# Optimization experiments

Hardware: AMD Instinct MI355X
Metric: run time of the kernel (lower is better)

Reference implementation:

```python
import jax, jax.numpy as jnp
import numpy as np

B, T, D, DFF = 8, 2048, 1024, 4096
EPS = 1e-6
PLIF_ALPHA = 2.0


@jax.custom_vjp
def spike_fn(m):
    # hard threshold forward, atan surrogate backward (PLIF neuron)
    return (m > 0.0).astype(m.dtype)

def _spk_fwd(m):
    return (m > 0.0).astype(m.dtype), m

def _spk_bwd(m, g):
    ds = PLIF_ALPHA / (2.0 * (1.0 + (jnp.pi * 0.5 * PLIF_ALPHA * m) ** 2))
    return (g * ds,)

spike_fn.defvjp(_spk_fwd, _spk_bwd)


def _rmsnorm(x, w):
    rstd = jax.lax.rsqrt(jnp.mean(x * x, axis=-1, keepdims=True) + EPS)
    return x * rstd * w


def setup_inputs() -> dict:
    key = jax.random.key(0)
    ks = jax.random.split(key, 9)
    sc = 0.02
    return {
        'x': jax.random.normal(ks[0], (B, T, D), jnp.float32),
        'rms_w1': jnp.ones((D,), jnp.float32),
        'rms_w2': jnp.ones((D,), jnp.float32),
        'delta_w': sc * jax.random.normal(ks[1], (D, D), jnp.float32),
        'delta_b': jnp.zeros((D,), jnp.float32),
        'b_w': sc * jax.random.normal(ks[2], (D, D), jnp.float32),
        'b_b': jnp.zeros((D,), jnp.float32),
        'A_log': jnp.log(jnp.linspace(0.5, 2.0, D).astype(jnp.float32)),
        'log_tau': jnp.full((D,), jnp.log(2.0), jnp.float32),
        'plif_thr': jnp.ones((D,), jnp.float32),
        'syn_w': sc * jax.random.normal(ks[3], (D, D), jnp.float32),
        'syn_b': jnp.zeros((D,), jnp.float32),
        'gate_w': sc * jax.random.normal(ks[4], (D, D), jnp.float32),
        'gate_b': jnp.zeros((D,), jnp.float32),
        'ffn_g_w': sc * jax.random.normal(ks[5], (DFF, D), jnp.float32),
        'ffn_u_w': sc * jax.random.normal(ks[6], (DFF, D), jnp.float32),
        'ffn_d_w': sc * jax.random.normal(ks[7], (D, DFF), jnp.float32),
    }


def _forward(x, rms_w1, rms_w2, delta_w, delta_b, b_w, b_b, A_log, log_tau,
             plif_thr, syn_w, syn_b, gate_w, gate_b, ffn_g_w, ffn_u_w, ffn_d_w):
    Bx, Tx, Dx = x.shape
    # --- RMSNorm 1 ---
    y1 = _rmsnorm(x, rms_w1)
    # --- selective-scan style liquid inputs ---
    delta = jax.nn.softplus(jnp.einsum('btd,ed->bte', y1, delta_w) + delta_b)  # [B,T,D]
    bvec = delta * (jnp.einsum('btd,ed->bte', y1, b_w) + b_b)                  # [B,T,D]
    A = jnp.exp(-delta * jnp.exp(A_log))                                        # [B,T,D]

    # --- liquid recurrent scan: h_t = tanh(A_t * h_{t-1} + b_t) ---
    def liquid_step(h, ab):
        a_t, b_t = ab
        h = jnp.tanh(a_t * h + b_t)
        return h, h

    h0 = jnp.zeros((Bx, Dx), x.dtype)
    _, h_post = jax.lax.scan(liquid_step, h0,
                             (jnp.swapaxes(A, 0, 1), jnp.swapaxes(bvec, 0, 1)))
    h_post = jnp.swapaxes(h_post, 0, 1)  # [B,T,D]

    # --- PLIF spiking scan with soft reset ---
    pdec = jnp.exp(-1.0 / jnp.exp(log_tau))  # [D]

    def plif_step(v, h_t):
        v_pre = pdec * v + (1.0 - pdec) * h_t
        s = spike_fn(v_pre - plif_thr)
        return v_pre - s * plif_thr, s

    v0 = jnp.zeros((Bx, Dx), x.dtype)
    _, spike = jax.lax.scan(plif_step, v0, jnp.swapaxes(h_post, 0, 1))
    spike = jnp.swapaxes(spike, 0, 1)

    # --- SEW shortcut + synaptic gate ---
    spike_in = spike + h_post
    syn = jnp.einsum('btd,ed->bte', spike_in, syn_w) + syn_b
    gate = jax.nn.sigmoid(jnp.einsum('btd,ed->bte', spike_in, gate_w) + gate_b)
    x1 = x + syn * gate

    # --- RMSNorm 2 + SwiGLU FFN + residual ---
    y2 = _rmsnorm(x1, rms_w2)
    ffn_act = jax.nn.silu(y2 @ ffn_g_w.T) * (y2 @ ffn_u_w.T)
    return x1 + ffn_act @ ffn_d_w.T


def reference(x, rms_w1, rms_w2, delta_w, delta_b, b_w, b_b, A_log, log_tau,
              plif_thr, syn_w, syn_b, gate_w, gate_b, ffn_g_w, ffn_u_w, ffn_d_w):
    return _forward(x, rms_w1, rms_w2, delta_w, delta_b, b_w, b_b, A_log,
                    log_tau, plif_thr, syn_w, syn_b, gate_w, gate_b,
                    ffn_g_w, ffn_u_w, ffn_d_w)
```

## Files before the change

kernel.cpp:

```cpp
#include <hip/hip_runtime.h>
#include <stdint.h>

#define B_   8
#define T_   2048
#define D_   1024
#define DFF_ 4096
#define M_   (B_ * T_)

typedef __bf16 bf16;
typedef bf16  bf16x8 __attribute__((ext_vector_type(8)));
typedef bf16  bf16x4 __attribute__((ext_vector_type(4)));
typedef float f32x4  __attribute__((ext_vector_type(4)));

#define CAST_LDS(p) ((__attribute__((address_space(3))) void*)(p))
#define CAST_GLB(p) ((const __attribute__((address_space(1))) void*)(p))

__global__ void f2bf_kernel(const float* __restrict__ s, bf16* __restrict__ d, int n) {
    int i = (blockIdx.x * 256 + threadIdx.x) * 4;
    if (i >= n) return;
    float4 v = *(const float4*)(s + i);
    bf16x4 o;
    o[0] = (bf16)v.x; o[1] = (bf16)v.y; o[2] = (bf16)v.z; o[3] = (bf16)v.w;
    *(bf16x4*)(d + i) = o;
}

__global__ __launch_bounds__(256) void rmsnorm_kernel(const float* __restrict__ x,
                                                      const float* __restrict__ w,
                                                      bf16* __restrict__ y) {
    const size_t row = blockIdx.x;
    const int t = threadIdx.x;
    const float4 v = ((const float4*)(x + row * D_))[t];
    float ss = v.x * v.x + v.y * v.y + v.z * v.z + v.w * v.w;
#pragma unroll
    for (int off = 32; off; off >>= 1) ss += __shfl_down(ss, off);
    __shared__ float red[4];
    if ((t & 63) == 0) red[t >> 6] = ss;
    __syncthreads();
    const float total = red[0] + red[1] + red[2] + red[3];
    const float rstd = rsqrtf(total * (1.0f / (float)D_) + 1e-6f);
    const float4 wv = ((const float4*)w)[t];
    bf16x4 o;
    o[0] = (bf16)(v.x * rstd * wv.x);
    o[1] = (bf16)(v.y * rstd * wv.y);
    o[2] = (bf16)(v.z * rstd * wv.z);
    o[3] = (bf16)(v.w * rstd * wv.w);
    ((bf16x4*)(y + row * D_))[t] = o;
}

#define SCAN_C  16
#define SCAN_L  (T_ / SCAN_C)
#define SCAN_W  64
#define SCAN_PF 8

template <int N, int W0>
__device__ __forceinline__ void scan_body(const uint32_t* __restrict__ p,
                                          bf16* __restrict__ o, const int ts,
                                          const float pdec, const float om,
                                          const float th) {
    uint32_t buf[SCAN_PF];
#pragma unroll
    for (int i = 0; i < SCAN_PF; ++i) buf[i] = p[(size_t)i * D_];
    float h = 0.0f, v = 0.0f;
#pragma unroll 8
    for (int k = 0; k < N; ++k) {
        const uint32_t w = buf[k & (SCAN_PF - 1)];
        if (k + SCAN_PF < N) buf[k & (SCAN_PF - 1)] = p[(size_t)(k + SCAN_PF) * D_];
        const float a  = __builtin_bit_cast(float, w << 16);
        const float bb = __builtin_bit_cast(float, w & 0xffff0000u);
        const float xv = fmaf(a, h, bb);
        const float e2 = __expf(2.0f * xv);
        h = 1.0f - __fdividef(2.0f, 1.0f + e2);
        const float vpre = fmaf(pdec, v, om * h);
        const float s = (vpre > th) ? 1.0f : 0.0f;
        v = vpre - s * th;
        if (k >= W0) o[(size_t)(ts + k) * D_] = (bf16)(s + h);
    }
}

__global__ __launch_bounds__(256) void scan_kernel(const uint32_t* __restrict__ ABp,
                                                   const float* __restrict__ log_tau,
                                                   const float* __restrict__ thr,
                                                   bf16* __restrict__ sp) {
    const int g = blockIdx.x * 256 + threadIdx.x;
    const int d = g & (D_ - 1);
    const int bc = g >> 10;
    const int b = bc >> 4;
    const int c = bc & (SCAN_C - 1);
    const float pdec = __expf(-__expf(-log_tau[d]));
    const float om = 1.0f - pdec;
    const float th = thr[d];
    const int t0 = c * SCAN_L;
    const uint32_t* base = ABp + (size_t)b * (T_ * D_) + d;
    bf16* o = sp + (size_t)b * (T_ * D_) + d;
    if (c == 0) {
        scan_body<SCAN_L, 0>(base, o, 0, pdec, om, th);
    } else {
        const int ts = t0 - SCAN_W;
        scan_body<SCAN_L + SCAN_W, SCAN_W>(base + (size_t)ts * D_, o, ts, pdec, om, th);
    }
}

template <int NB, int MODE>
__global__ __launch_bounds__(256, 2) void gemm_kernel(
    const bf16* __restrict__ A, const bf16* __restrict__ W1, const bf16* __restrict__ W2,
    const int M, const int N, const int K,
    const float* __restrict__ b1, const float* __restrict__ b2,
    const float* __restrict__ extra, void* __restrict__ outp) {
    __shared__ bf16 As[128 * 32];
    __shared__ bf16 Bs[NB][128 * 32];

    const int tid = threadIdx.x;
    const int wave = tid >> 6;
    const int lane = tid & 63;
    const int lane15 = lane & 15;
    const int quad = lane >> 4;
    const int m0 = blockIdx.y * 128;
    const int n0 = blockIdx.x * 128;
    const int wm = (wave >> 1) * 64;
    const int wn = (wave & 1) * 64;

    f32x4 acc[NB][4][4] = {};

    const int srow = lane >> 2;
    const int scol = (lane & 3) * 8;
    const bf16* gA = A + (size_t)(m0 + wave * 32 + srow) * K + scol;
    const bf16* gW[2];
    gW[0] = W1 + (size_t)(n0 + wave * 32 + srow) * K + scol;
    if (NB > 1) gW[1] = W2 + (size_t)(n0 + wave * 32 + srow) * K + scol;

    bf16* lA = As + (wave * 32) * 32;

    for (int k0 = 0; k0 < K; k0 += 32) {
        __builtin_amdgcn_global_load_lds(CAST_GLB(gA + k0),            CAST_LDS(lA),            16, 0, 0);
        __builtin_amdgcn_global_load_lds(CAST_GLB(gA + k0 + 16 * K),   CAST_LDS(lA + 16 * 32),  16, 0, 0);
#pragma unroll
        for (int nb = 0; nb < NB; ++nb) {
            bf16* lB = &Bs[nb][(wave * 32) * 32];
            __builtin_amdgcn_global_load_lds(CAST_GLB(gW[nb] + k0),          CAST_LDS(lB),           16, 0, 0);
            __builtin_amdgcn_global_load_lds(CAST_GLB(gW[nb] + k0 + 16 * K), CAST_LDS(lB + 16 * 32), 16, 0, 0);
        }
        __syncthreads();

        bf16x8 af[4];
#pragma unroll
        for (int i = 0; i < 4; ++i)
            af[i] = *(const bf16x8*)(As + (wm + i * 16 + lane15) * 32 + quad * 8);
#pragma unroll
        for (int nb = 0; nb < NB; ++nb) {
#pragma unroll
            for (int j = 0; j < 4; ++j) {
                const bf16x8 bfj = *(const bf16x8*)(&Bs[nb][(wn + j * 16 + lane15) * 32 + quad * 8]);
#pragma unroll
                for (int i = 0; i < 4; ++i)
                    acc[nb][i][j] = __builtin_amdgcn_mfma_f32_16x16x32_bf16(af[i], bfj, acc[nb][i][j], 0, 0, 0);
            }
        }
        __syncthreads();
    }

#pragma unroll
    for (int i = 0; i < 4; ++i) {
#pragma unroll
        for (int r = 0; r < 4; ++r) {
            const int m = m0 + wm + i * 16 + quad * 4 + r;
#pragma unroll
            for (int j = 0; j < 4; ++j) {
                const int n = n0 + wn + j * 16 + lane15;
                const size_t idx = (size_t)m * N + n;
                const float v1 = acc[0][i][j][r];
                if constexpr (MODE == 0) {
                    const float v2 = acc[1][i][j][r];
                    const float dl = v1 + b1[n];
                    const float spv = (dl > 20.0f) ? dl : log1pf(__expf(dl));
                    const float bv = spv * (v2 + b2[n]);
                    const float av = __expf(-spv * __expf(extra[n]));
                    const uint32_t pa = (uint32_t)__builtin_bit_cast(unsigned short, (bf16)av);
                    const uint32_t pb = (uint32_t)__builtin_bit_cast(unsigned short, (bf16)bv);
                    ((uint32_t*)outp)[idx] = pa | (pb << 16);
                } else if constexpr (MODE == 1) {
                    const float v2 = acc[1][i][j][r];
                    const float syn = v1 + b1[n];
                    const float z = v2 + b2[n];
                    const float gate = 1.0f / (1.0f + __expf(-z));
                    ((float*)outp)[idx] = extra[idx] + syn * gate;
                } else if constexpr (MODE == 2) {
                    const float v2 = acc[1][i][j][r];
                    const float sg = v1 / (1.0f + __expf(-v1));
                    ((bf16*)outp)[idx] = (bf16)(sg * v2);
                } else {
                    ((float*)outp)[idx] = extra[idx] + v1;
                }
            }
        }
    }
}

extern "C" void kernel_launch(void* const* d_in, const int* in_sizes, int n_in,
                              void* d_out, int out_size, void* d_ws, size_t ws_size,
                              hipStream_t stream) {
    const float* x        = (const float*)d_in[0];
    const float* rms_w1   = (const float*)d_in[1];
    const float* rms_w2   = (const float*)d_in[2];
    const float* delta_w  = (const float*)d_in[3];
    const float* delta_b  = (const float*)d_in[4];
    const float* b_w      = (const float*)d_in[5];
    const float* b_b      = (const float*)d_in[6];
    const float* A_log    = (const float*)d_in[7];
    const float* log_tau  = (const float*)d_in[8];
    const float* plif_thr = (const float*)d_in[9];
    const float* syn_w    = (const float*)d_in[10];
    const float* syn_b    = (const float*)d_in[11];
    const float* gate_w   = (const float*)d_in[12];
    const float* gate_b   = (const float*)d_in[13];
    const float* ffn_g_w  = (const float*)d_in[14];
    const float* ffn_u_w  = (const float*)d_in[15];
    const float* ffn_d_w  = (const float*)d_in[16];

    char* ws = (char*)d_ws;
    const size_t MB = 1024ull * 1024ull;
    bf16* wdelta = (bf16*)(ws + 0 * MB);
    bf16* wb     = (bf16*)(ws + 2 * MB);
    bf16* wsyn   = (bf16*)(ws + 4 * MB);
    bf16* wgate  = (bf16*)(ws + 6 * MB);
    bf16* wg     = (bf16*)(ws + 8 * MB);
    bf16* wu     = (bf16*)(ws + 16 * MB);
    bf16* wd     = (bf16*)(ws + 24 * MB);
    bf16*     y1      = (bf16*)(ws + 32 * MB);
    uint32_t* ABp     = (uint32_t*)(ws + 64 * MB);
    bf16*     spikein = (bf16*)(ws + 128 * MB);
    float* x1 = (float*)(ws + 160 * MB);
    bf16*  y2 = (bf16*)(ws + 224 * MB);
    bf16* act = (bf16*)(ws + 32 * MB);
    float* outF = (float*)d_out;

    const int DD = D_ * D_;
    const int DF = DFF_ * D_;

    f2bf_kernel<<<DD / 1024, 256, 0, stream>>>(delta_w, wdelta, DD);
    f2bf_kernel<<<DD / 1024, 256, 0, stream>>>(b_w, wb, DD);
    f2bf_kernel<<<DD / 1024, 256, 0, stream>>>(syn_w, wsyn, DD);
    f2bf_kernel<<<DD / 1024, 256, 0, stream>>>(gate_w, wgate, DD);
    f2bf_kernel<<<DF / 1024, 256, 0, stream>>>(ffn_g_w, wg, DF);
    f2bf_kernel<<<DF / 1024, 256, 0, stream>>>(ffn_u_w, wu, DF);
    f2bf_kernel<<<DF / 1024, 256, 0, stream>>>(ffn_d_w, wd, DF);

    rmsnorm_kernel<<<M_, 256, 0, stream>>>(x, rms_w1, y1);

    gemm_kernel<2, 0><<<dim3(D_ / 128, M_ / 128), 256, 0, stream>>>(
        y1, wdelta, wb, M_, D_, D_, delta_b, b_b, A_log, ABp);

    scan_kernel<<<(B_ * SCAN_C * D_) / 256, 256, 0, stream>>>(ABp, log_tau, plif_thr, spikein);

    gemm_kernel<2, 1><<<dim3(D_ / 128, M_ / 128), 256, 0, stream>>>(
        spikein, wsyn, wgate, M_, D_, D_, syn_b, gate_b, x, x1);

    rmsnorm_kernel<<<M_, 256, 0, stream>>>(x1, rms_w2, y2);

    gemm_kernel<2, 2><<<dim3(DFF_ / 128, M_ / 128), 256, 0, stream>>>(
        y2, wg, wu, M_, DFF_, D_, nullptr, nullptr, nullptr, act);

    gemm_kernel<1, 3><<<dim3(D_ / 128, M_ / 128), 256, 0, stream>>>(
        act, wd, nullptr, M_, D_, DFF_, nullptr, nullptr, x1, outF);
}
```

Before: 1.028 ms.

## Swizzle GEMM LDS tiles and merge weight conversions into one launch

Applies an XOR swizzle to the 16-byte column chunks of the A and B tiles in LDS. Both the global-to-LDS loads and the fragment reads use it, so the MFMA operand loads hit fewer LDS bank conflicts. Separately, the seven fp32-to-bf16 weight conversion launches become one kernel that picks its segment from cumulative block counts, which cuts launch overhead. The swizzle must match on the load and read sides or the results are wrong.

```diff
diff --git a/kernel.cpp b/kernel.cpp
--- a/kernel.cpp
+++ b/kernel.cpp
@@ -15,13 +15,23 @@
 #define CAST_LDS(p) ((__attribute__((address_space(3))) void*)(p))
 #define CAST_GLB(p) ((const __attribute__((address_space(1))) void*)(p))
 
-__global__ void f2bf_kernel(const float* __restrict__ s, bf16* __restrict__ d, int n) {
-    int i = (blockIdx.x * 256 + threadIdx.x) * 4;
-    if (i >= n) return;
-    float4 v = *(const float4*)(s + i);
+struct CvtArgs {
+    const float* s[7];
+    bf16* d[7];
+    int nblk[7];
+};
+
+__global__ __launch_bounds__(256) void f2bf_all_kernel(CvtArgs a) {
+    int blk = blockIdx.x;
+    int seg = 0;
+#pragma unroll
+    for (int i = 0; i < 7; ++i) seg += (blk >= a.nblk[i]) ? 1 : 0;
+    const int base = (seg == 0) ? 0 : a.nblk[seg - 1];
+    const int i = ((blk - base) * 256 + threadIdx.x) * 4;
+    const float4 v = *(const float4*)(a.s[seg] + i);
     bf16x4 o;
     o[0] = (bf16)v.x; o[1] = (bf16)v.y; o[2] = (bf16)v.z; o[3] = (bf16)v.w;
-    *(bf16x4*)(d + i) = o;
+    *(bf16x4*)(a.d[seg] + i) = o;
 }
 
 __global__ __launch_bounds__(256) void rmsnorm_kernel(const float* __restrict__ x,
@@ -122,13 +132,15 @@
     f32x4 acc[NB][4][4] = {};
 
     const int srow = lane >> 2;
-    const int scol = (lane & 3) * 8;
+    const int scol = (((lane & 3) ^ (srow & 3)) * 8);
     const bf16* gA = A + (size_t)(m0 + wave * 32 + srow) * K + scol;
     const bf16* gW[2];
     gW[0] = W1 + (size_t)(n0 + wave * 32 + srow) * K + scol;
     if (NB > 1) gW[1] = W2 + (size_t)(n0 + wave * 32 + srow) * K + scol;
 
     bf16* lA = As + (wave * 32) * 32;
+
+    const int rq = (quad ^ (lane15 & 3)) * 8;
 
     for (int k0 = 0; k0 < K; k0 += 32) {
         __builtin_amdgcn_global_load_lds(CAST_GLB(gA + k0),            CAST_LDS(lA),            16, 0, 0);
@@ -144,12 +156,12 @@
         bf16x8 af[4];
 #pragma unroll
         for (int i = 0; i < 4; ++i)
-            af[i] = *(const bf16x8*)(As + (wm + i * 16 + lane15) * 32 + quad * 8);
+            af[i] = *(const bf16x8*)(As + (wm + i * 16 + lane15) * 32 + rq);
 #pragma unroll
         for (int nb = 0; nb < NB; ++nb) {
 #pragma unroll
             for (int j = 0; j < 4; ++j) {
-                const bf16x8 bfj = *(const bf16x8*)(&Bs[nb][(wn + j * 16 + lane15) * 32 + quad * 8]);
+                const bf16x8 bfj = *(const bf16x8*)(&Bs[nb][(wn + j * 16 + lane15) * 32 + rq]);
 #pragma unroll
                 for (int i = 0; i < 4; ++i)
                     acc[nb][i][j] = __builtin_amdgcn_mfma_f32_16x16x32_bf16(af[i], bfj, acc[nb][i][j], 0, 0, 0);
@@ -235,14 +247,21 @@
 
     const int DD = D_ * D_;
     const int DF = DFF_ * D_;
-
-    f2bf_kernel<<<DD / 1024, 256, 0, stream>>>(delta_w, wdelta, DD);
-    f2bf_kernel<<<DD / 1024, 256, 0, stream>>>(b_w, wb, DD);
-    f2bf_kernel<<<DD / 1024, 256, 0, stream>>>(syn_w, wsyn, DD);
-    f2bf_kernel<<<DD / 1024, 256, 0, stream>>>(gate_w, wgate, DD);
-    f2bf_kernel<<<DF / 1024, 256, 0, stream>>>(ffn_g_w, wg, DF);
-    f2bf_kernel<<<DF / 1024, 256, 0, stream>>>(ffn_u_w, wu, DF);
-    f2bf_kernel<<<DF / 1024, 256, 0, stream>>>(ffn_d_w, wd, DF);
+    const int BD = DD / 1024;
+    const int BF = DF / 1024;
+
+    CvtArgs ca;
+    ca.s[0] = delta_w; ca.d[0] = wdelta;
+    ca.s[1] = b_w;     ca.d[1] = wb;
+    ca.s[2] = syn_w;   ca.d[2] = wsyn;
+    ca.s[3] = gate_w;  ca.d[3] = wgate;
+    ca.s[4] = ffn_g_w; ca.d[4] = wg;
+    ca.s[5] = ffn_u_w; ca.d[5] = wu;
+    ca.s[6] = ffn_d_w; ca.d[6] = wd;
+    int acc_blk = 0;
+    const int segblk[7] = {BD, BD, BD, BD, BF, BF, BF};
+    for (int i = 0; i < 7; ++i) { acc_blk += segblk[i]; ca.nblk[i] = acc_blk; }
+    f2bf_all_kernel<<<acc_blk, 256, 0, stream>>>(ca);
 
     rmsnorm_kernel<<<M_, 256, 0, stream>>>(x, rms_w1, y1);
 
```

Result: slower. 1.126 ms (+9.5%).
